# Kernel tuning notes

Hardware: AMD Instinct MI355X
Metric: run time of the kernel (lower is better)

Reference implementation:

```python
import jax, jax.numpy as jnp
import numpy as np

B_, L_, DM = 8, 1024, 256
DS, DC, EX = 16, 4, 2
DI = EX * DM            # d_inner = 512
DTR = max(1, DM // 16)  # dt_rank = 16


def setup_inputs() -> dict:
    key = jax.random.key(0)
    ks = iter(jax.random.split(key, 40))
    def n(shape, s=0.02):
        return jax.random.normal(next(ks), shape, jnp.float32) * s
    inp = {"x": jax.random.normal(next(ks), (B_, L_, DM), jnp.float32)}
    inp["norm_g"] = jnp.ones((DM,), jnp.float32)
    inp["norm_b"] = jnp.zeros((DM,), jnp.float32)
    for m in ("f", "b"):
        inp[f"inW_{m}"] = n((DM, 2 * DI))
        inp[f"convW_{m}"] = n((DI, DC))
        inp[f"convB_{m}"] = jnp.zeros((DI,), jnp.float32)
        inp[f"xW_{m}"] = n((DI, DTR + 2 * DS))
        inp[f"dtW_{m}"] = n((DTR, DI))
        inp[f"dtB_{m}"] = jnp.zeros((DI,), jnp.float32)
        # ALog init: log of [1..dState] repeated over dInner rows
        inp[f"ALog_{m}"] = jnp.log(jnp.tile(jnp.arange(1, DS + 1, dtype=jnp.float32), (DI, 1)))
        inp[f"Dp_{m}"] = jnp.ones((DI,), jnp.float32)
        inp[f"outW_{m}"] = n((DI, DM))
    inp["fusW"] = n((2 * DM, DM))
    inp["fusB"] = jnp.zeros((DM,), jnp.float32)
    return inp


def _dw_conv(x, w, b):
    # causal depthwise conv1d: x [B,L,DI], w [DI,DC] -> [B,L,DI]
    xc = jnp.transpose(x, (0, 2, 1))  # B,DI,L
    out = jax.lax.conv_general_dilated(
        xc, w[:, None, :], window_strides=(1,), padding=[(DC - 1, 0)],
        dimension_numbers=("NCH", "OIH", "NCH"), feature_group_count=DI)
    return jnp.transpose(out + b[:, None], (0, 2, 1))


def _ssm(x, xW, dtW, dtB, ALog, Dp):
    # x: [B,L,DI]
    A = -jnp.exp(ALog)                                   # [DI,DS]
    xdbl = x @ xW                                        # [B,L,DTR+2*DS]
    dlt, Bp, Cp = jnp.split(xdbl, [DTR, DTR + DS], axis=-1)
    delta = jax.nn.softplus(dlt @ dtW + dtB)             # [B,L,DI]
    dA = jnp.exp(delta[..., None] * A)                   # [B,L,DI,DS]
    dBx = (delta * x)[..., None] * Bp[:, :, None, :]     # [B,L,DI,DS]

    def step(h, t):
        a, bb, c = t
        h = a * h + bb                                   # [B,DI,DS]
        y = jnp.einsum('bdn,bn->bd', h, c)
        return h, y

    h0 = jnp.zeros((x.shape[0], DI, DS), x.dtype)
    _, ys = jax.lax.scan(step, h0, (jnp.moveaxis(dA, 1, 0),
                                    jnp.moveaxis(dBx, 1, 0),
                                    jnp.moveaxis(Cp, 1, 0)))
    return jnp.moveaxis(ys, 0, 1) + Dp * x               # [B,L,DI]


def _mamba(x, inW, convW, convB, xW, dtW, dtB, ALog, Dp, outW):
    xr = x @ inW                                         # [B,L,2*DI]
    xs, res = jnp.split(xr, 2, axis=-1)
    xs = jax.nn.silu(_dw_conv(xs, convW, convB))
    y = _ssm(xs, xW, dtW, dtB, ALog, Dp)
    return (y * jax.nn.silu(res)) @ outW                 # [B,L,DM]


def reference(x, norm_g, norm_b,
              inW_f, convW_f, convB_f, xW_f, dtW_f, dtB_f, ALog_f, Dp_f, outW_f,
              inW_b, convW_b, convB_b, xW_b, dtW_b, dtB_b, ALog_b, Dp_b, outW_b,
              fusW, fusB):
    # LayerNorm
    mu = x.mean(-1, keepdims=True)
    var = ((x - mu) ** 2).mean(-1, keepdims=True)
    xn = (x - mu) * jax.lax.rsqrt(var + 1e-5) * norm_g + norm_b
    # forward-direction Mamba
    xf = _mamba(xn, inW_f, convW_f, convB_f, xW_f, dtW_f, dtB_f, ALog_f, Dp_f, outW_f)
    # backward-direction Mamba (flip along time)
    xb = _mamba(jnp.flip(xn, 1), inW_b, convW_b, convB_b, xW_b, dtW_b, dtB_b, ALog_b, Dp_b, outW_b)
    xb = jnp.flip(xb, 1)
    fused = jnp.concatenate([xf, xb], axis=-1) @ fusW + fusB
    return x + fused  # dropout is identity in eval
```

## Files before the change

### kernel.cpp

```cpp
#include <hip/hip_runtime.h>
#include <cmath>

typedef __bf16 bf16x8 __attribute__((ext_vector_type(8)));
typedef float  f32x4  __attribute__((ext_vector_type(4)));
typedef float  f32x2  __attribute__((ext_vector_type(2)));

#define B_  8
#define L_  1024
#define DM  256
#define DI  512
#define DS  16
#define DTR 16
#define M_  (B_*L_)
#define NC  64
#define CT  16

__device__ inline float softplus_f(float z){
  return (z > 20.f) ? z : __logf(1.f + __expf(z));
}
__device__ inline float silu_f(float z){
  return z / (1.f + __expf(-z));
}

__device__ inline void pow_tree(float e1, float* p){
  float e2=e1*e1, e4=e2*e2, e8=e4*e4;
  float e3=e2*e1, e5=e4*e1, e6=e4*e2, e7=e4*e3;
  p[0]=e1;  p[1]=e2;  p[2]=e3;  p[3]=e4;
  p[4]=e5;  p[5]=e6;  p[6]=e7;  p[7]=e8;
  p[8]=e8*e1;  p[9]=e8*e2;  p[10]=e8*e3;  p[11]=e8*e4;
  p[12]=e8*e5; p[13]=e8*e6; p[14]=e8*e7;  p[15]=e8*e8;
}

__global__ __launch_bounds__(256) void probe_k(const void* x, int* flag){
  __shared__ int sbad[256];
  int tid = threadIdx.x;
  const unsigned short* u = (const unsigned short*)x;
  int bad = 0;
  for (int i = tid; i < 4096; i += 256){
    unsigned short v = u[2*i];
    int e = (v >> 7) & 0xFF;
    if (e >= 160 || e < 96) bad++;
  }
  sbad[tid] = bad;
  __syncthreads();
  if (tid == 0){
    int t = 0;
    for (int i=0;i<256;i++) t += sbad[i];
    *flag = (t > 1024) ? 1 : 0;
  }
}

struct CvtJob { const void* src; __bf16* dst; int n; };
struct CvtArgs { CvtJob j[11]; };

__global__ __launch_bounds__(256) void cvt_k(CvtArgs a, const int* flag){
  int e = blockIdx.x*256 + threadIdx.x;
  const int f = *flag;
  #pragma unroll 1
  for (int jj=0; jj<11; jj++){
    int n = a.j[jj].n;
    if (e < n){
      if (f) a.j[jj].dst[e] = (__bf16)(((const float*)a.j[jj].src)[e]);
      else   a.j[jj].dst[e] = ((const __bf16*)a.j[jj].src)[e];
      return;
    }
    e -= n;
  }
}

__global__ __launch_bounds__(256) void cvtA_k(const void* a0, const void* a1,
                                              float* o0, float* o1, const int* flag){
  int gid = blockIdx.x*256 + threadIdx.x;
  const int f = *flag;
  const void* src = (gid < 8192) ? a0 : a1;
  float* dst = (gid < 8192) ? o0 : o1;
  int i = gid & 8191;
  dst[i] = f ? ((const float*)src)[i] : (float)((const __bf16*)src)[i];
}

struct PrepJob { const void* src; void* dst; int rows; int cols; int f32out; };
struct PrepArgs { PrepJob j[11]; };

__global__ __launch_bounds__(256) void prep_k(PrepArgs a, const int* flag){
  int e = blockIdx.x*256 + threadIdx.x;
  const int f = *flag;
  #pragma unroll 1
  for (int jj=0; jj<11; jj++){
    int sz = a.j[jj].rows * a.j[jj].cols;
    if (e < sz){
      int cols = a.j[jj].cols;
      int r = e / cols, c = e - r*cols;
      float v = f ? ((const float*)a.j[jj].src)[e] : (float)((const __bf16*)a.j[jj].src)[e];
      if (a.j[jj].f32out) ((float*)a.j[jj].dst)[c*a.j[jj].rows + r] = v;
      else ((__bf16*)a.j[jj].dst)[(long)c*a.j[jj].rows + r] = (__bf16)v;
      return;
    }
    e -= sz;
  }
}

__global__ __launch_bounds__(256) void ln_k(const void* x, const __bf16* g,
                                            const __bf16* bb, __bf16* xn, const int* flag){
  const int row = blockIdx.x;
  const int d = threadIdx.x;
  const int f = *flag;
  long idx = (long)row*DM + d;
  float v = f ? ((const float*)x)[idx] : (float)(((const __bf16*)x)[idx]);
  float s = v, q = v*v;
  #pragma unroll
  for (int off=32; off>0; off>>=1){
    s += __shfl_down(s, off);
    q += __shfl_down(q, off);
  }
  __shared__ float ss[4], sq[4];
  int w = d >> 6, ln = d & 63;
  if (ln == 0){ ss[w] = s; sq[w] = q; }
  __syncthreads();
  s = ss[0]+ss[1]+ss[2]+ss[3];
  q = sq[0]+sq[1]+sq[2]+sq[3];
  float mu  = s * (1.f/DM);
  float var = q * (1.f/DM) - mu*mu;
  float xnv = (v - mu) * rsqrtf(var + 1e-5f) * (float)g[d] + (float)bb[d];
  xn[idx] = (__bf16)xnv;
}

template<int BM,int BN,int EPI,int KK>
__global__ __launch_bounds__(256) void gemm_lds_k(
    const __bf16* A0, const __bf16* A1,
    const __bf16* B0, const __bf16* B1,
    void* C0, void* C1,
    int lda, int ldb, int ldc,
    const __bf16* bias, const void* resid, const int* outflag)
{
  constexpr int TM = BM/2, TN = BN/2;
  constexpr int WMT = TM/16, WNT = TN/16;
  constexpr int LA = BM/64, LB = BN/64;

  const int dir = blockIdx.z;
  const __bf16* A  = dir ? A1 : A0;
  const __bf16* Bt = dir ? B1 : B0;
  char* C = (char*)(dir ? C1 : C0);
  __bf16* resW = (EPI==0) ? (__bf16*)(dir ? resid : (const void*)bias) : nullptr;
  const int tid  = threadIdx.x;
  const int lane = tid & 63;
  const int wid  = tid >> 6;
  const int wm = wid & 1;
  const int wn = wid >> 1;
  const int mBase = blockIdx.x * BM;
  const int nBase = blockIdx.y * BN;
  const int lm = lane & 15;
  const int kq = (lane >> 4) * 8;
  const int of = (EPI==3 && outflag) ? *outflag : 0;

  __shared__ __bf16 As[BM*32];
  __shared__ __bf16 Bs[BN*32];

  const __bf16* aS[LA];
  const __bf16* bS[LB];
  {
    int colk = (tid & 3) * 8;
    #pragma unroll
    for (int ld=0; ld<LA; ld++){
      int r = mBase + ld*64 + (tid >> 2);
      if (EPI==0 && dir==1){ int b = r >> 10, t = r & (L_-1); r = (b<<10) + (L_-1-t); }
      aS[ld] = A + (long)r*lda + colk;
    }
    #pragma unroll
    for (int ld=0; ld<LB; ld++){
      int r = nBase + ld*64 + (tid >> 2);
      bS[ld] = Bt + (long)r*ldb + colk;
    }
  }

  f32x4 acc[WMT][WNT] = {};
  for (int k0=0; k0<KK; k0+=32){
    #pragma unroll
    for (int ld=0; ld<LA; ld++)
      __builtin_amdgcn_global_load_lds(
        (const __attribute__((address_space(1))) void*)(aS[ld] + k0),
        (__attribute__((address_space(3))) void*)(&As[ld*2048 + tid*8]), 16, 0, 0);
    #pragma unroll
    for (int ld=0; ld<LB; ld++)
      __builtin_amdgcn_global_load_lds(
        (const __attribute__((address_space(1))) void*)(bS[ld] + k0),
        (__attribute__((address_space(3))) void*)(&Bs[ld*2048 + tid*8]), 16, 0, 0);
    __syncthreads();
    bf16x8 af[WMT], bfr[WNT];
    #pragma unroll
    for (int i=0;i<WMT;i++) af[i]  = *(const bf16x8*)&As[(wm*TM + i*16 + lm)*32 + kq];
    #pragma unroll
    for (int j=0;j<WNT;j++) bfr[j] = *(const bf16x8*)&Bs[(wn*TN + j*16 + lm)*32 + kq];
    #pragma unroll
    for (int i=0;i<WMT;i++)
      #pragma unroll
      for (int j=0;j<WNT;j++)
        acc[i][j] = __builtin_amdgcn_mfma_f32_16x16x32_bf16(af[i], bfr[j], acc[i][j], 0,0,0);
    __syncthreads();
  }

  const int coff = (EPI==2) ? dir*DM : 0;
  #pragma unroll
  for (int i=0;i<WMT;i++){
    #pragma unroll
    for (int rr=0;rr<4;rr++){
      int r = mBase + wm*TM + i*16 + (lane>>4)*4 + rr;
      int rOut = r;
      if (EPI==2 && dir==1){ int b = r >> 10, t = r & (L_-1); rOut = (b<<10) + (L_-1-t); }
      #pragma unroll
      for (int j=0;j<WNT;j++){
        int c = nBase + wn*TN + j*16 + lm;
        float v = acc[i][j][rr];
        if (EPI==0){
          if (c < DI) ((__bf16*)C)[(long)r*DI + c] = (__bf16)v;
          else        resW[(long)r*DI + (c-DI)]    = (__bf16)v;
        } else if (EPI==3){
          float rsd = of ? ((const float*)resid)[(long)r*DM + c]
                         : (float)((const __bf16*)resid)[(long)r*DM + c];
          v += (float)bias[c] + rsd;
          if (of) ((float*)C)[(long)r*ldc + c] = v;
          else    ((__bf16*)C)[(long)r*ldc + c] = (__bf16)v;
        } else {
          ((__bf16*)C)[(long)rOut*ldc + coff + c] = (__bf16)v;
        }
      }
    }
  }
}

template<int WMT,int WNT,int BWM,int BWN,int KK>
__global__ __launch_bounds__(64*BWM*BWN) void gemm_r_k(
    const __bf16* A0, const __bf16* A1,
    const __bf16* B0, const __bf16* B1,
    float* C0, float* C1,
    int lda, int ldb, int ldc)
{
  const int dir = blockIdx.z;
  const __bf16* A  = dir ? A1 : A0;
  const __bf16* Bt = dir ? B1 : B0;
  float* C = dir ? C1 : C0;
  const int tid  = threadIdx.x;
  const int lane = tid & 63;
  const int wid  = tid >> 6;
  const int wm = wid % BWM;
  const int wn = wid / BWM;
  const int mBase = (blockIdx.x*BWM + wm) * (WMT*16);
  const int nBase = (blockIdx.y*BWN + wn) * (WNT*16);
  const int lm = lane & 15;
  const int kq = (lane >> 4) * 8;

  long aoff[WMT];
  #pragma unroll
  for (int i=0;i<WMT;i++) aoff[i] = (long)(mBase + i*16 + lm) * lda + kq;
  long boff[WNT];
  #pragma unroll
  for (int j=0;j<WNT;j++) boff[j] = (long)(nBase + j*16 + lm) * ldb + kq;

  f32x4 acc[WMT][WNT] = {};
  #pragma unroll
  for (int k0=0; k0<KK; k0+=32){
    bf16x8 af[WMT], bfr[WNT];
    #pragma unroll
    for (int i=0;i<WMT;i++) af[i]  = *(const bf16x8*)(A  + aoff[i] + k0);
    #pragma unroll
    for (int j=0;j<WNT;j++) bfr[j] = *(const bf16x8*)(Bt + boff[j] + k0);
    #pragma unroll
    for (int i=0;i<WMT;i++)
      #pragma unroll
      for (int j=0;j<WNT;j++)
        acc[i][j] = __builtin_amdgcn_mfma_f32_16x16x32_bf16(af[i], bfr[j], acc[i][j], 0,0,0);
  }

  #pragma unroll
  for (int i=0;i<WMT;i++)
    #pragma unroll
    for (int rr=0;rr<4;rr++){
      int r = mBase + i*16 + (lane>>4)*4 + rr;
      #pragma unroll
      for (int j=0;j<WNT;j++){
        int c = nBase + j*16 + lm;
        C[(long)r*ldc + c] = acc[i][j][rr];
      }
    }
}

__global__ __launch_bounds__(256) void conv_k(
    const __bf16* xz0, const __bf16* xz1,
    const float* cw0, const float* cw1,
    const __bf16* cb0, const __bf16* cb1,
    __bf16* xs0, __bf16* xs1)
{
  const int dir = blockIdx.z;
  const __bf16* xz = dir ? xz1 : xz0;
  const float*  cw = dir ? cw1 : cw0;
  const __bf16* cb = dir ? cb1 : cb0;
  __bf16* xs = dir ? xs1 : xs0;

  int gid = blockIdx.x*256 + threadIdx.x;
  int c8 = gid & 63;
  int t  = (gid >> 6) & (L_-1);
  int b  = gid >> 16;
  int cbase = c8*8;

  float acc[8];
  bf16x8 bb = *(const bf16x8*)(cb + cbase);
  #pragma unroll
  for (int c=0;c<8;c++) acc[c] = (float)bb[c];
  #pragma unroll
  for (int j=0;j<4;j++){
    int tj = t - 3 + j;
    if (tj >= 0){
      bf16x8 xv = *(const bf16x8*)(xz + ((long)(b*L_ + tj))*DI + cbase);
      #pragma unroll
      for (int c=0;c<8;c++) acc[c] += (float)xv[c] * cw[j*DI + cbase + c];
    }
  }
  bf16x8 outv;
  #pragma unroll
  for (int c=0;c<8;c++) outv[c] = (__bf16)silu_f(acc[c]);
  *(bf16x8*)(xs + ((long)(b*L_ + t))*DI + cbase) = outv;
}

__global__ __launch_bounds__(256) void dt_k(
    const float* xd0, const float* xd1,
    const float* dw0, const float* dw1,
    const __bf16* dtB0, const __bf16* dtB1,
    float* dg0, float* dg1)
{
  const int dir = blockIdx.z;
  const float*  xd  = dir ? xd1 : xd0;
  const float*  dw  = dir ? dw1 : dw0;
  const __bf16* dtB = dir ? dtB1 : dtB0;
  float* dg = dir ? dg1 : dg0;
  const long row0 = (long)blockIdx.x * 32;
  const int tid = threadIdx.x;

  __shared__ float sdlt[32][16];
  { int e = tid*2; int r = e>>4, q = e&15;
    *(f32x2*)&sdlt[r][q] = *(const f32x2*)(xd + (row0+r)*48 + q); }

  const int d0 = tid, d1 = tid + 256;
  float dwa[16], dwb[16];
  { const f32x4* p = (const f32x4*)(dw + d0*DTR);
    #pragma unroll
    for (int q=0;q<4;q++){ f32x4 v=p[q]; dwa[q*4]=v[0]; dwa[q*4+1]=v[1]; dwa[q*4+2]=v[2]; dwa[q*4+3]=v[3]; } }
  { const f32x4* p = (const f32x4*)(dw + d1*DTR);
    #pragma unroll
    for (int q=0;q<4;q++){ f32x4 v=p[q]; dwb[q*4]=v[0]; dwb[q*4+1]=v[1]; dwb[q*4+2]=v[2]; dwb[q*4+3]=v[3]; } }
  const float b0v = (float)dtB[d0];
  const float b1v = (float)dtB[d1];
  __syncthreads();

  #pragma unroll 4
  for (int r=0;r<32;r++){
    f32x4 q0 = *(const f32x4*)&sdlt[r][0];
    f32x4 q1 = *(const f32x4*)&sdlt[r][4];
    f32x4 q2 = *(const f32x4*)&sdlt[r][8];
    f32x4 q3 = *(const f32x4*)&sdlt[r][12];
    float z0 = b0v, z1 = b1v;
    z0 += q0[0]*dwa[0]+q0[1]*dwa[1]+q0[2]*dwa[2]+q0[3]*dwa[3];
    z0 += q1[0]*dwa[4]+q1[1]*dwa[5]+q1[2]*dwa[6]+q1[3]*dwa[7];
    z0 += q2[0]*dwa[8]+q2[1]*dwa[9]+q2[2]*dwa[10]+q2[3]*dwa[11];
    z0 += q3[0]*dwa[12]+q3[1]*dwa[13]+q3[2]*dwa[14]+q3[3]*dwa[15];
    z1 += q0[0]*dwb[0]+q0[1]*dwb[1]+q0[2]*dwb[2]+q0[3]*dwb[3];
    z1 += q1[0]*dwb[4]+q1[1]*dwb[5]+q1[2]*dwb[6]+q1[3]*dwb[7];
    z1 += q2[0]*dwb[8]+q2[1]*dwb[9]+q2[2]*dwb[10]+q2[3]*dwb[11];
    z1 += q3[0]*dwb[12]+q3[1]*dwb[13]+q3[2]*dwb[14]+q3[3]*dwb[15];
    dg[(row0+r)*DI + d0] = softplus_f(z0);
    dg[(row0+r)*DI + d1] = softplus_f(z1);
  }
}

__global__ __launch_bounds__(256) void scanA_k(
    const float* xd0, const float* xd1,
    const __bf16* xs0, const __bf16* xs1,
    const float* dg0, const float* dg1,
    const float* ALf0, const float* ALf1,
    float* hend, float* sumd)
{
  const int dir = blockIdx.z;
  const float*  xd  = dir ? xd1 : xd0;
  const __bf16* xs  = dir ? xs1 : xs0;
  const float*  dg  = dir ? dg1 : dg0;
  const float*  ALf = dir ? ALf1 : ALf0;

  const int b   = blockIdx.y;
  const int c   = blockIdx.x >> 1;
  const int dg_ = blockIdx.x & 1;
  const int tid = threadIdx.x;
  const int d   = dg_*256 + tid;
  const int db  = dir*8 + b;
  const long row0 = (long)b*L_ + c*CT;

  __shared__ float sB[CT][16];
  if (tid < CT*4){ int e = tid*4; int t = e>>4, n = e&15;
    *(f32x4*)&sB[t][n] = *(const f32x4*)(xd + (row0+t)*48 + 16 + n); }

  float A[16];
  { const f32x4* p = (const f32x4*)(ALf + d*DS);
    #pragma unroll
    for (int q=0;q<4;q++){ f32x4 v=p[q];
      A[q*4]=-__expf(v[0]); A[q*4+1]=-__expf(v[1]); A[q*4+2]=-__expf(v[2]); A[q*4+3]=-__expf(v[3]); } }
  bool pow_ok = true;
  #pragma unroll
  for (int n=0;n<16;n++) pow_ok = pow_ok && (fabsf(A[n] + (float)(n+1)) < 0.003f*(n+1));

  float h[16];
  #pragma unroll
  for (int n=0;n<16;n++) h[n]=0.f;
  float sdelta = 0.f;
  __syncthreads();

  if (pow_ok){
    #pragma unroll 2
    for (int t=0;t<CT;t++){
      long row = row0 + t;
      f32x4 b0 = *(const f32x4*)&sB[t][0];
      f32x4 b1 = *(const f32x4*)&sB[t][4];
      f32x4 b2 = *(const f32x4*)&sB[t][8];
      f32x4 b3 = *(const f32x4*)&sB[t][12];
      float delta = dg[row*DI + d];
      sdelta += delta;
      float xv = (float)xs[row*DI + d];
      float dx = delta*xv;
      float pw[16];
      pow_tree(__expf(-delta), pw);
      float Bv[16] = {b0[0],b0[1],b0[2],b0[3], b1[0],b1[1],b1[2],b1[3],
                      b2[0],b2[1],b2[2],b2[3], b3[0],b3[1],b3[2],b3[3]};
      #pragma unroll
      for (int n=0;n<16;n++)
        h[n] = pw[n]*h[n] + dx*Bv[n];
    }
  } else {
    #pragma unroll 2
    for (int t=0;t<CT;t++){
      long row = row0 + t;
      f32x4 b0 = *(const f32x4*)&sB[t][0];
      f32x4 b1 = *(const f32x4*)&sB[t][4];
      f32x4 b2 = *(const f32x4*)&sB[t][8];
      f32x4 b3 = *(const f32x4*)&sB[t][12];
      float delta = dg[row*DI + d];
      sdelta += delta;
      float xv = (float)xs[row*DI + d];
      float dx = delta*xv;
      float Bv[16] = {b0[0],b0[1],b0[2],b0[3], b1[0],b1[1],b1[2],b1[3],
                      b2[0],b2[1],b2[2],b2[3], b3[0],b3[1],b3[2],b3[3]};
      #pragma unroll
      for (int n=0;n<16;n++)
        h[n] = __expf(delta*A[n])*h[n] + dx*Bv[n];
    }
  }

  long hb = (((long)db*NC + c)*DI + d)*16;
  f32x4* hp = (f32x4*)(hend + hb);
  #pragma unroll
  for (int q=0;q<4;q++){ f32x4 v; v[0]=h[q*4]; v[1]=h[q*4+1]; v[2]=h[q*4+2]; v[3]=h[q*4+3]; hp[q]=v; }
  sumd[((long)db*NC + c)*DI + d] = sdelta;
}

__global__ __launch_bounds__(256) void scanB_k(
    const float* ALf0, const float* ALf1,
    const float* hend, const float* sumd, float* Hbuf)
{
  int gid = blockIdx.x*256 + threadIdx.x;
  int n  = gid & 15;
  int d  = (gid>>4) & 511;
  int db = gid >> 13;
  const float* ALf = (db>=8) ? ALf1 : ALf0;
  float A_dn = -__expf(ALf[d*DS + n]);
  float H = 0.f;
  #pragma unroll 1
  for (int c=0;c<NC;c++){
    long base = (((long)db*NC + c)*DI + d)*16 + n;
    Hbuf[base] = H;
    float S = sumd[((long)db*NC + c)*DI + d];
    H = hend[base] + __expf(A_dn*S)*H;
  }
}

__global__ __launch_bounds__(256) void scanC_k(
    const float* xd0, const float* xd1,
    const __bf16* xs0, const __bf16* xs1,
    __bf16* res0, __bf16* res1,
    const float* dg0, const float* dg1,
    const float* ALf0, const float* ALf1,
    const __bf16* Dp0, const __bf16* Dp1,
    const float* Hbuf)
{
  const int dir = blockIdx.z;
  const float*  xd  = dir ? xd1 : xd0;
  const __bf16* xs  = dir ? xs1 : xs0;
  __bf16*       res = dir ? res1 : res0;
  const float*  dg  = dir ? dg1 : dg0;
  const float*  ALf = dir ? ALf1 : ALf0;
  const __bf16* Dp  = dir ? Dp1 : Dp0;

  const int b   = blockIdx.y;
  const int c   = blockIdx.x >> 1;
  const int dg_ = blockIdx.x & 1;
  const int tid = threadIdx.x;
  const int d   = dg_*256 + tid;
  const int db  = dir*8 + b;
  const long row0 = (long)b*L_ + c*CT;

  __shared__ float sBC[CT][32];
  if (tid < CT*8){ int e = tid*4; int t = e>>5, cc = e&31;
    *(f32x4*)&sBC[t][cc] = *(const f32x4*)(xd + (row0+t)*48 + 16 + cc); }

  float A[16];
  { const f32x4* p = (const f32x4*)(ALf + d*DS);
    #pragma unroll
    for (int q=0;q<4;q++){ f32x4 v=p[q];
      A[q*4]=-__expf(v[0]); A[q*4+1]=-__expf(v[1]); A[q*4+2]=-__expf(v[2]); A[q*4+3]=-__expf(v[3]); } }
  bool pow_ok = true;
  #pragma unroll
  for (int n=0;n<16;n++) pow_ok = pow_ok && (fabsf(A[n] + (float)(n+1)) < 0.003f*(n+1));

  float h[16];
  { long hb = (((long)db*NC + c)*DI + d)*16;
    const f32x4* p = (const f32x4*)(Hbuf + hb);
    #pragma unroll
    for (int q=0;q<4;q++){ f32x4 v = p[q]; h[q*4]=v[0]; h[q*4+1]=v[1]; h[q*4+2]=v[2]; h[q*4+3]=v[3]; } }
  const float Dpv = (float)Dp[d];
  __syncthreads();

  if (pow_ok){
    #pragma unroll 2
    for (int t=0;t<CT;t++){
      long row = row0 + t;
      f32x4 b0 = *(const f32x4*)&sBC[t][0];
      f32x4 b1 = *(const f32x4*)&sBC[t][4];
      f32x4 b2 = *(const f32x4*)&sBC[t][8];
      f32x4 b3 = *(const f32x4*)&sBC[t][12];
      f32x4 c0 = *(const f32x4*)&sBC[t][16];
      f32x4 c1 = *(const f32x4*)&sBC[t][20];
      f32x4 c2 = *(const f32x4*)&sBC[t][24];
      f32x4 c3 = *(const f32x4*)&sBC[t][28];
      float delta = dg[row*DI + d];
      float xv = (float)xs[row*DI + d];
      float dx = delta*xv;
      float pw[16];
      pow_tree(__expf(-delta), pw);
      float Bv[16] = {b0[0],b0[1],b0[2],b0[3], b1[0],b1[1],b1[2],b1[3],
                      b2[0],b2[1],b2[2],b2[3], b3[0],b3[1],b3[2],b3[3]};
      float Cv[16] = {c0[0],c0[1],c0[2],c0[3], c1[0],c1[1],c1[2],c1[3],
                      c2[0],c2[1],c2[2],c2[3], c3[0],c3[1],c3[2],c3[3]};
      float p = 0.f;
      #pragma unroll
      for (int n=0;n<16;n++){
        h[n] = pw[n]*h[n] + dx*Bv[n];
        p += h[n]*Cv[n];
      }
      float yv = p + Dpv*xv;
      float rv = (float)res[row*DI + d];
      res[row*DI + d] = (__bf16)(yv * silu_f(rv));
    }
  } else {
    #pragma unroll 2
    for (int t=0;t<CT;t++){
      long row = row0 + t;
      f32x4 b0 = *(const f32x4*)&sBC[t][0];
      f32x4 b1 = *(const f32x4*)&sBC[t][4];
      f32x4 b2 = *(const f32x4*)&sBC[t][8];
      f32x4 b3 = *(const f32x4*)&sBC[t][12];
      f32x4 c0 = *(const f32x4*)&sBC[t][16];
      f32x4 c1 = *(const f32x4*)&sBC[t][20];
      f32x4 c2 = *(const f32x4*)&sBC[t][24];
      f32x4 c3 = *(const f32x4*)&sBC[t][28];
      float delta = dg[row*DI + d];
      float xv = (float)xs[row*DI + d];
      float dx = delta*xv;
      float Bv[16] = {b0[0],b0[1],b0[2],b0[3], b1[0],b1[1],b1[2],b1[3],
                      b2[0],b2[1],b2[2],b2[3], b3[0],b3[1],b3[2],b3[3]};
      float Cv[16] = {c0[0],c0[1],c0[2],c0[3], c1[0],c1[1],c1[2],c1[3],
                      c2[0],c2[1],c2[2],c2[3], c3[0],c3[1],c3[2],c3[3]};
      float p = 0.f;
      #pragma unroll
      for (int n=0;n<16;n++){
        h[n] = __expf(delta*A[n])*h[n] + dx*Bv[n];
        p += h[n]*Cv[n];
      }
      float yv = p + Dpv*xv;
      float rv = (float)res[row*DI + d];
      res[row*DI + d] = (__bf16)(yv * silu_f(rv));
    }
  }
}

__global__ __launch_bounds__(256) void scan_k(
    const float* xd0, const float* xd1,
    const __bf16* xs0, const __bf16* xs1,
    __bf16* res0, __bf16* res1,
    const float* dw0, const float* dw1,
    const __bf16* dtB0, const __bf16* dtB1,
    const __bf16* AL0, const __bf16* AL1,
    const __bf16* Dp0, const __bf16* Dp1)
{
  const int dir = blockIdx.z;
  const float*  xd  = dir ? xd1 : xd0;
  const __bf16* xs  = dir ? xs1 : xs0;
  __bf16*       res = dir ? res1 : res0;
  const float*  dw  = dir ? dw1 : dw0;
  const __bf16* dtB = dir ? dtB1 : dtB0;
  const __bf16* AL  = dir ? AL1 : AL0;
  const __bf16* Dp  = dir ? Dp1 : Dp0;

  const int b  = blockIdx.y;
  const int dt = blockIdx.x;
  const int tid = threadIdx.x;
  const int n  = tid & 15;
  const int dl = tid >> 4;
  const int d  = dt*16 + dl;

  __shared__ float sxd[128][48];
  __shared__ float sx[128][16];
  __shared__ float sdelta[128][16];
  __shared__ float sy[128][16];
  __shared__ float sdw[16][17];
  __shared__ float sdb[16];

  sdw[dl][n] = dw[(dt*16+dl)*DTR + n];
  if (tid < 16) sdb[tid] = (float)dtB[dt*16 + tid];
  const float A_dn = -__expf((float)AL[d*DS + n]);
  float h = 0.f;
  __syncthreads();

  const long rowB = (long)b * L_;
  for (int c0=0; c0<L_; c0+=128){
    #pragma unroll 1
    for (int k=0;k<24;k++){
      int e = tid + k*256;
      int t = e / 48, col = e - t*48;
      sxd[t][col] = xd[(rowB + c0 + t)*48 + col];
    }
    #pragma unroll 1
    for (int k=0;k<8;k++){
      int e = tid + k*256;
      int t = e >> 4, dc = e & 15;
      sx[t][dc] = (float)xs[(rowB + c0 + t)*DI + dt*16 + dc];
    }
    __syncthreads();
    #pragma unroll 1
    for (int k=0;k<8;k++){
      int e = tid + k*256;
      int t = e >> 4, dc = e & 15;
      float z = sdb[dc];
      #pragma unroll
      for (int q=0;q<16;q++) z += sxd[t][q] * sdw[dc][q];
      sdelta[t][dc] = softplus_f(z);
    }
    __syncthreads();
    #pragma unroll 2
    for (int tt=0;tt<128;tt++){
      float delta = sdelta[tt][dl];
      float xv = sx[tt][dl];
      float Bv = sxd[tt][16+n];
      float Cv = sxd[tt][32+n];
      float dA = __expf(delta * A_dn);
      h = dA*h + (delta*xv)*Bv;
      float p = h * Cv;
      p += __shfl_xor(p, 1);
      p += __shfl_xor(p, 2);
      p += __shfl_xor(p, 4);
      p += __shfl_xor(p, 8);
      if (n == 0) sy[tt][dl] = p;
    }
    __syncthreads();
    #pragma unroll 1
    for (int k=0;k<8;k++){
      int e = tid + k*256;
      int t = e >> 4, dc = e & 15;
      long row = rowB + c0 + t;
      float yv = sy[t][dc] + (float)Dp[dt*16+dc] * sx[t][dc];
      float rv = (float)res[row*DI + dt*16 + dc];
      res[row*DI + dt*16 + dc] = (__bf16)(yv * silu_f(rv));
    }
    __syncthreads();
  }
}

extern "C" void kernel_launch(void* const* d_in, const int* in_sizes, int n_in,
                              void* d_out, int out_size, void* d_ws, size_t ws_size,
                              hipStream_t stream)
{
  const size_t MB = 1u<<20;
  if (ws_size < 61*MB) return;
  const bool newscan = (ws_size >= 160*MB);

  char* w = (char*)d_ws;
  __bf16* xz[2]  = {(__bf16*)(w + 0),      (__bf16*)(w + 8*MB)};
  __bf16* res[2] = {(__bf16*)(w + 16*MB),  (__bf16*)(w + 24*MB)};
  __bf16* xsc[2] = {(__bf16*)(w + 32*MB),  (__bf16*)(w + 40*MB)};
  __bf16* xn     = (__bf16*)(w + 48*MB);
  float*  xdbl[2]= {(float*)(w + 48*MB),   (float*)(w + 48*MB + (size_t)M_*48*4)};
  __bf16* fusedIn = xsc[0];

  char* wp = w + 52*MB;
  auto carve = [&](size_t bytes)->void*{
    void* p = wp;
    wp += (bytes + 255) & ~(size_t)255;
    return p;
  };
  __bf16 *inWt[2], *xWt[2], *outWt[2];
  float *dtWt[2], *convWt[2];
  for (int m=0;m<2;m++){
    inWt[m]   = (__bf16*)carve((size_t)(2*DI)*DM*2);
    xWt[m]    = (__bf16*)carve((size_t)48*DI*2);
    outWt[m]  = (__bf16*)carve((size_t)DM*DI*2);
    dtWt[m]   = (float*)carve((size_t)DI*DTR*4);
    convWt[m] = (float*)carve((size_t)4*DI*4);
  }
  __bf16* fusWt = (__bf16*)carve((size_t)DM*DI*2);
  int* flag = (int*)carve(256);
  float* ALf[2] = {(float*)carve((size_t)DI*DS*4), (float*)carve((size_t)DI*DS*4)};

  char* cp = w + 55*MB;
  auto carve2 = [&](size_t elems)->__bf16*{
    __bf16* p = (__bf16*)cp;
    cp += (elems*2 + 255) & ~(size_t)255;
    return p;
  };
  __bf16* ngc = carve2(DM);
  __bf16* nbc = carve2(DM);
  __bf16 *convBc[2], *dtBc[2], *ALc[2], *Dpc[2];
  for (int m=0;m<2;m++){
    convBc[m] = carve2(DI);
    dtBc[m]   = carve2(DI);
    ALc[m]    = carve2((size_t)DI*DS);
    Dpc[m]    = carve2(DI);
  }
  __bf16* fusBc = carve2(DM);

  float* dgA[2] = {(float*)(w + 56*MB), (float*)(w + 72*MB)};
  float* hend = (float*)(w + 88*MB);
  float* sumd = (float*)(w + 122*MB);
  float* Hbuf = (float*)(w + 125*MB);

  probe_k<<<1, 256, 0, stream>>>(d_in[0], flag);

  CvtArgs ca;
  int ci = 0;
  ca.j[ci++] = {d_in[1],  ngc, DM};
  ca.j[ci++] = {d_in[2],  nbc, DM};
  for (int m=0;m<2;m++){
    int base = 3 + m*9;
    ca.j[ci++] = {d_in[base+2], convBc[m], DI};
    ca.j[ci++] = {d_in[base+5], dtBc[m],   DI};
    ca.j[ci++] = {d_in[base+6], ALc[m],    DI*DS};
    ca.j[ci++] = {d_in[base+7], Dpc[m],    DI};
  }
  ca.j[ci++] = {d_in[22], fusBc, DM};
  cvt_k<<<79, 256, 0, stream>>>(ca, flag);
  cvtA_k<<<64, 256, 0, stream>>>(d_in[9], d_in[18], ALf[0], ALf[1], flag);

  PrepArgs pa;
  int ji = 0;
  for (int m=0;m<2;m++){
    int base = 3 + m*9;
    pa.j[ji++] = {d_in[base+0], inWt[m],  DM,  2*DI, 0};
    pa.j[ji++] = {d_in[base+3], xWt[m],   DI,  48,   0};
    pa.j[ji++] = {d_in[base+8], outWt[m], DI,  DM,   0};
    pa.j[ji++] = {d_in[base+4], dtWt[m],  DTR, DI,   1};
    pa.j[ji++] = {d_in[base+1], convWt[m],DI,  4,    1};
  }
  pa.j[ji++] = {d_in[21], fusWt, DI, DM, 0};
  prep_k<<<(987136+255)/256, 256, 0, stream>>>(pa, flag);

  ln_k<<<M_, 256, 0, stream>>>(d_in[0], ngc, nbc, xn, flag);
  gemm_lds_k<128,128,0,256><<<dim3(M_/128, (2*DI)/128, 2), 256, 0, stream>>>(
      xn, xn, inWt[0], inWt[1], xz[0], xz[1], DM, DM, DI, res[0], res[1], nullptr);
  conv_k<<<dim3((M_*64)/256, 1, 2), 256, 0, stream>>>(
      xz[0], xz[1], convWt[0], convWt[1], convBc[0], convBc[1], xsc[0], xsc[1]);
  gemm_r_k<1,3,4,1,512><<<dim3(M_/64, 1, 2), 256, 0, stream>>>(
      xsc[0], xsc[1], xWt[0], xWt[1], xdbl[0], xdbl[1], DI, DI, 48);

  if (newscan){
    dt_k<<<dim3(M_/32, 1, 2), 256, 0, stream>>>(
        xdbl[0], xdbl[1], dtWt[0], dtWt[1], dtBc[0], dtBc[1], dgA[0], dgA[1]);
    scanA_k<<<dim3(NC*2, B_, 2), 256, 0, stream>>>(
        xdbl[0], xdbl[1], xsc[0], xsc[1], dgA[0], dgA[1], ALf[0], ALf[1], hend, sumd);
    scanB_k<<<131072/256, 256, 0, stream>>>(ALf[0], ALf[1], hend, sumd, Hbuf);
    scanC_k<<<dim3(NC*2, B_, 2), 256, 0, stream>>>(
        xdbl[0], xdbl[1], xsc[0], xsc[1], res[0], res[1],
        dgA[0], dgA[1], ALf[0], ALf[1], Dpc[0], Dpc[1], Hbuf);
  } else {
    scan_k<<<dim3(DI/16, B_, 2), 256, 0, stream>>>(
        xdbl[0], xdbl[1], xsc[0], xsc[1], res[0], res[1], dtWt[0], dtWt[1],
        dtBc[0], dtBc[1], ALc[0], ALc[1], Dpc[0], Dpc[1]);
  }

  gemm_lds_k<64,64,2,512><<<dim3(M_/64, DM/64, 2), 256, 0, stream>>>(
      res[0], res[1], outWt[0], outWt[1], fusedIn, fusedIn, DI, DI, 2*DM, nullptr, nullptr, nullptr);
  gemm_lds_k<64,64,3,512><<<dim3(M_/64, DM/64, 1), 256, 0, stream>>>(
      fusedIn, fusedIn, fusWt, fusWt, d_out, d_out, 2*DM, 2*DM, DM, fusBc, d_in[0], flag);
}
```

Baseline: 286.3 us.

## Fold out-projection into fusion weights and merge conversion kernels

Precomputes the product of each direction's out-projection with its half of the fusion weight (outW·fusW) using a small GEMM. The final stage then becomes a single GEMM that accumulates both directions' gated SSM outputs over K=512 each against the combined weights, with the backward direction's time flip handled at load. This removes the intermediate fusedIn tensor and one large GEMM launch. The separate cvt/cvtA kernels are folded into the generalized prep kernel. The combined weights are rounded to bf16, which changes numerics slightly.

After: 283.4 us. No clear change (-1.0%).

```diff
diff --git a/kernel.cpp b/kernel.cpp
--- a/kernel.cpp
+++ b/kernel.cpp
@@ -50,42 +50,14 @@
   }
 }
 
-struct CvtJob { const void* src; __bf16* dst; int n; };
-struct CvtArgs { CvtJob j[11]; };
-
-__global__ __launch_bounds__(256) void cvt_k(CvtArgs a, const int* flag){
-  int e = blockIdx.x*256 + threadIdx.x;
-  const int f = *flag;
-  #pragma unroll 1
-  for (int jj=0; jj<11; jj++){
-    int n = a.j[jj].n;
-    if (e < n){
-      if (f) a.j[jj].dst[e] = (__bf16)(((const float*)a.j[jj].src)[e]);
-      else   a.j[jj].dst[e] = ((const __bf16*)a.j[jj].src)[e];
-      return;
-    }
-    e -= n;
-  }
-}
-
-__global__ __launch_bounds__(256) void cvtA_k(const void* a0, const void* a1,
-                                              float* o0, float* o1, const int* flag){
-  int gid = blockIdx.x*256 + threadIdx.x;
-  const int f = *flag;
-  const void* src = (gid < 8192) ? a0 : a1;
-  float* dst = (gid < 8192) ? o0 : o1;
-  int i = gid & 8191;
-  dst[i] = f ? ((const float*)src)[i] : (float)((const __bf16*)src)[i];
-}
-
 struct PrepJob { const void* src; void* dst; int rows; int cols; int f32out; };
-struct PrepArgs { PrepJob j[11]; };
+struct PrepArgs { PrepJob j[26]; int nj; };
 
 __global__ __launch_bounds__(256) void prep_k(PrepArgs a, const int* flag){
   int e = blockIdx.x*256 + threadIdx.x;
   const int f = *flag;
   #pragma unroll 1
-  for (int jj=0; jj<11; jj++){
+  for (int jj=0; jj<a.nj; jj++){
     int sz = a.j[jj].rows * a.j[jj].cols;
     if (e < sz){
       int cols = a.j[jj].cols;
@@ -124,23 +96,20 @@
   xn[idx] = (__bf16)xnv;
 }
 
-template<int BM,int BN,int EPI,int KK>
-__global__ __launch_bounds__(256) void gemm_lds_k(
-    const __bf16* A0, const __bf16* A1,
-    const __bf16* B0, const __bf16* B1,
-    void* C0, void* C1,
-    int lda, int ldb, int ldc,
-    const __bf16* bias, const void* resid, const int* outflag)
+template<int BM,int BN,int KK>
+__global__ __launch_bounds__(256) void gemm_in_k(
+    const __bf16* A, const __bf16* B0, const __bf16* B1,
+    __bf16* xz0, __bf16* xz1, __bf16* res0, __bf16* res1,
+    int lda, int ldb)
 {
   constexpr int TM = BM/2, TN = BN/2;
   constexpr int WMT = TM/16, WNT = TN/16;
   constexpr int LA = BM/64, LB = BN/64;
 
   const int dir = blockIdx.z;
-  const __bf16* A  = dir ? A1 : A0;
   const __bf16* Bt = dir ? B1 : B0;
-  char* C = (char*)(dir ? C1 : C0);
-  __bf16* resW = (EPI==0) ? (__bf16*)(dir ? resid : (const void*)bias) : nullptr;
+  __bf16* xz  = dir ? xz1 : xz0;
+  __bf16* res = dir ? res1 : res0;
   const int tid  = threadIdx.x;
   const int lane = tid & 63;
   const int wid  = tid >> 6;
@@ -150,7 +119,6 @@
   const int nBase = blockIdx.y * BN;
   const int lm = lane & 15;
   const int kq = (lane >> 4) * 8;
-  const int of = (EPI==3 && outflag) ? *outflag : 0;
 
   __shared__ __bf16 As[BM*32];
   __shared__ __bf16 Bs[BN*32];
@@ -162,7 +130,7 @@
     #pragma unroll
     for (int ld=0; ld<LA; ld++){
       int r = mBase + ld*64 + (tid >> 2);
-      if (EPI==0 && dir==1){ int b = r >> 10, t = r & (L_-1); r = (b<<10) + (L_-1-t); }
+      if (dir==1){ int b = r >> 10, t = r & (L_-1); r = (b<<10) + (L_-1-t); }
       aS[ld] = A + (long)r*lda + colk;
     }
     #pragma unroll
@@ -198,46 +166,123 @@
     __syncthreads();
   }
 
-  const int coff = (EPI==2) ? dir*DM : 0;
   #pragma unroll
   for (int i=0;i<WMT;i++){
     #pragma unroll
     for (int rr=0;rr<4;rr++){
       int r = mBase + wm*TM + i*16 + (lane>>4)*4 + rr;
-      int rOut = r;
-      if (EPI==2 && dir==1){ int b = r >> 10, t = r & (L_-1); rOut = (b<<10) + (L_-1-t); }
       #pragma unroll
       for (int j=0;j<WNT;j++){
         int c = nBase + wn*TN + j*16 + lm;
         float v = acc[i][j][rr];
-        if (EPI==0){
-          if (c < DI) ((__bf16*)C)[(long)r*DI + c] = (__bf16)v;
-          else        resW[(long)r*DI + (c-DI)]    = (__bf16)v;
-        } else if (EPI==3){
-          float rsd = of ? ((const float*)resid)[(long)r*DM + c]
-                         : (float)((const __bf16*)resid)[(long)r*DM + c];
-          v += (float)bias[c] + rsd;
-          if (of) ((float*)C)[(long)r*ldc + c] = v;
-          else    ((__bf16*)C)[(long)r*ldc + c] = (__bf16)v;
-        } else {
-          ((__bf16*)C)[(long)rOut*ldc + coff + c] = (__bf16)v;
-        }
+        if (c < DI) xz[(long)r*DI + c] = (__bf16)v;
+        else        res[(long)r*DI + (c-DI)] = (__bf16)v;
       }
     }
   }
 }
 
-template<int WMT,int WNT,int BWM,int BWN,int KK>
+template<int BM,int BN,int KK>
+__global__ __launch_bounds__(256) void gemm_fin_k(
+    const __bf16* Af, const __bf16* Ab,
+    const __bf16* Bt0, const __bf16* Bt1,
+    void* Cout, const __bf16* bias, const void* resid, const int* outflag)
+{
+  constexpr int TM = BM/2, TN = BN/2;
+  constexpr int WMT = TM/16, WNT = TN/16;
+  constexpr int LA = BM/64, LB = BN/64;
+
+  const int tid  = threadIdx.x;
+  const int lane = tid & 63;
+  const int wid  = tid >> 6;
+  const int wm = wid & 1;
+  const int wn = wid >> 1;
+  const int mBase = blockIdx.x * BM;
+  const int nBase = blockIdx.y * BN;
+  const int lm = lane & 15;
+  const int kq = (lane >> 4) * 8;
+  const int of = outflag ? *outflag : 0;
+
+  __shared__ __bf16 As[BM*32];
+  __shared__ __bf16 Bs[BN*32];
+
+  f32x4 acc[WMT][WNT] = {};
+  #pragma unroll 1
+  for (int dd=0; dd<2; dd++){
+    const __bf16* A  = dd ? Ab  : Af;
+    const __bf16* Bt = dd ? Bt1 : Bt0;
+    const __bf16* aS[LA];
+    const __bf16* bS[LB];
+    {
+      int colk = (tid & 3) * 8;
+      #pragma unroll
+      for (int ld=0; ld<LA; ld++){
+        int r = mBase + ld*64 + (tid >> 2);
+        if (dd==1){ int b = r >> 10, t = r & (L_-1); r = (b<<10) + (L_-1-t); }
+        aS[ld] = A + (long)r*DI + colk;
+      }
+      #pragma unroll
+      for (int ld=0; ld<LB; ld++){
+        int r = nBase + ld*64 + (tid >> 2);
+        bS[ld] = Bt + (long)r*DI + colk;
+      }
+    }
+    for (int k0=0; k0<KK; k0+=32){
+      #pragma unroll
+      for (int ld=0; ld<LA; ld++)
+        __builtin_amdgcn_global_load_lds(
+          (const __attribute__((address_space(1))) void*)(aS[ld] + k0),
+          (__attribute__((address_space(3))) void*)(&As[ld*2048 + tid*8]), 16, 0, 0);
+      #pragma unroll
+      for (int ld=0; ld<LB; ld++)
+        __builtin_amdgcn_global_load_lds(
+          (const __attribute__((address_space(1))) void*)(bS[ld] + k0),
+          (__attribute__((address_space(3))) void*)(&Bs[ld*2048 + tid*8]), 16, 0, 0);
+      __syncthreads();
+      bf16x8 af[WMT], bfr[WNT];
+      #pragma unroll
+      for (int i=0;i<WMT;i++) af[i]  = *(const bf16x8*)&As[(wm*TM + i*16 + lm)*32 + kq];
+      #pragma unroll
+      for (int j=0;j<WNT;j++) bfr[j] = *(const bf16x8*)&Bs[(wn*TN + j*16 + lm)*32 + kq];
+      #pragma unroll
+      for (int i=0;i<WMT;i++)
+        #pragma unroll
+        for (int j=0;j<WNT;j++)
+          acc[i][j] = __builtin_amdgcn_mfma_f32_16x16x32_bf16(af[i], bfr[j], acc[i][j], 0,0,0);
+      __syncthreads();
+    }
+  }
+
+  #pragma unroll
+  for (int i=0;i<WMT;i++){
+    #pragma unroll
+    for (int rr=0;rr<4;rr++){
+      int r = mBase + wm*TM + i*16 + (lane>>4)*4 + rr;
+      #pragma unroll
+      for (int j=0;j<WNT;j++){
+        int c = nBase + wn*TN + j*16 + lm;
+        float v = acc[i][j][rr];
+        float rsd = of ? ((const float*)resid)[(long)r*DM + c]
+                       : (float)((const __bf16*)resid)[(long)r*DM + c];
+        v += (float)bias[c] + rsd;
+        if (of) ((float*)Cout)[(long)r*DM + c] = v;
+        else    ((__bf16*)Cout)[(long)r*DM + c] = (__bf16)v;
+      }
+    }
+  }
+}
+
+template<int WMT,int WNT,int BWM,int BWN,int KK,int BF16OUT>
 __global__ __launch_bounds__(64*BWM*BWN) void gemm_r_k(
     const __bf16* A0, const __bf16* A1,
     const __bf16* B0, const __bf16* B1,
-    float* C0, float* C1,
+    void* C0, void* C1,
     int lda, int ldb, int ldc)
 {
   const int dir = blockIdx.z;
   const __bf16* A  = dir ? A1 : A0;
   const __bf16* Bt = dir ? B1 : B0;
-  float* C = dir ? C1 : C0;
+  void* C = dir ? C1 : C0;
   const int tid  = threadIdx.x;
   const int lane = tid & 63;
   const int wid  = tid >> 6;
@@ -278,7 +323,8 @@
       #pragma unroll
       for (int j=0;j<WNT;j++){
         int c = nBase + j*16 + lm;
-        C[(long)r*ldc + c] = acc[i][j][rr];
+        if (BF16OUT) ((__bf16*)C)[(long)r*ldc + c] = (__bf16)acc[i][j][rr];
+        else         ((float*)C)[(long)r*ldc + c] = acc[i][j][rr];
       }
     }
 }
@@ -692,7 +738,6 @@
   __bf16* xsc[2] = {(__bf16*)(w + 32*MB),  (__bf16*)(w + 40*MB)};
   __bf16* xn     = (__bf16*)(w + 48*MB);
   float*  xdbl[2]= {(float*)(w + 48*MB),   (float*)(w + 48*MB + (size_t)M_*48*4)};
-  __bf16* fusedIn = xsc[0];
 
   char* wp = w + 52*MB;
   auto carve = [&](size_t bytes)->void*{
@@ -700,20 +745,21 @@
     wp += (bytes + 255) & ~(size_t)255;
     return p;
   };
-  __bf16 *inWt[2], *xWt[2], *outWt[2];
+  __bf16 *inWt[2], *xWt[2], *outWr[2], *BtC[2];
   float *dtWt[2], *convWt[2];
   for (int m=0;m<2;m++){
     inWt[m]   = (__bf16*)carve((size_t)(2*DI)*DM*2);
     xWt[m]    = (__bf16*)carve((size_t)48*DI*2);
-    outWt[m]  = (__bf16*)carve((size_t)DM*DI*2);
+    outWr[m]  = (__bf16*)carve((size_t)DI*DM*2);
+    BtC[m]    = (__bf16*)carve((size_t)DM*DI*2);
     dtWt[m]   = (float*)carve((size_t)DI*DTR*4);
     convWt[m] = (float*)carve((size_t)4*DI*4);
   }
-  __bf16* fusWt = (__bf16*)carve((size_t)DM*DI*2);
+  __bf16* fusWt = (__bf16*)carve((size_t)DM*(2*DM)*2);
   int* flag = (int*)carve(256);
   float* ALf[2] = {(float*)carve((size_t)DI*DS*4), (float*)carve((size_t)DI*DS*4)};
 
-  char* cp = w + 55*MB;
+  char* cp = w + 57*MB;
   auto carve2 = [&](size_t elems)->__bf16*{
     __bf16* p = (__bf16*)cp;
     cp += (elems*2 + 255) & ~(size_t)255;
@@ -730,47 +776,50 @@
   }
   __bf16* fusBc = carve2(DM);
 
-  float* dgA[2] = {(float*)(w + 56*MB), (float*)(w + 72*MB)};
-  float* hend = (float*)(w + 88*MB);
-  float* sumd = (float*)(w + 122*MB);
-  float* Hbuf = (float*)(w + 125*MB);
+  float* dgA[2] = {(float*)(w + 58*MB), (float*)(w + 74*MB)};
+  float* hend = (float*)(w + 90*MB);
+  float* sumd = (float*)(w + 124*MB);
+  float* Hbuf = (float*)(w + 127*MB);
 
   probe_k<<<1, 256, 0, stream>>>(d_in[0], flag);
 
-  CvtArgs ca;
-  int ci = 0;
-  ca.j[ci++] = {d_in[1],  ngc, DM};
-  ca.j[ci++] = {d_in[2],  nbc, DM};
+  PrepArgs pa;
+  int ji = 0;
+  size_t tot = 0;
+  auto addj = [&](const void* s, void* dst, int rows, int cols, int f32o){
+    pa.j[ji++] = {s, dst, rows, cols, f32o};
+    tot += (size_t)rows*cols;
+  };
   for (int m=0;m<2;m++){
     int base = 3 + m*9;
-    ca.j[ci++] = {d_in[base+2], convBc[m], DI};
-    ca.j[ci++] = {d_in[base+5], dtBc[m],   DI};
-    ca.j[ci++] = {d_in[base+6], ALc[m],    DI*DS};
-    ca.j[ci++] = {d_in[base+7], Dpc[m],    DI};
-  }
-  ca.j[ci++] = {d_in[22], fusBc, DM};
-  cvt_k<<<79, 256, 0, stream>>>(ca, flag);
-  cvtA_k<<<64, 256, 0, stream>>>(d_in[9], d_in[18], ALf[0], ALf[1], flag);
-
-  PrepArgs pa;
-  int ji = 0;
-  for (int m=0;m<2;m++){
-    int base = 3 + m*9;
-    pa.j[ji++] = {d_in[base+0], inWt[m],  DM,  2*DI, 0};
-    pa.j[ji++] = {d_in[base+3], xWt[m],   DI,  48,   0};
-    pa.j[ji++] = {d_in[base+8], outWt[m], DI,  DM,   0};
-    pa.j[ji++] = {d_in[base+4], dtWt[m],  DTR, DI,   1};
-    pa.j[ji++] = {d_in[base+1], convWt[m],DI,  4,    1};
-  }
-  pa.j[ji++] = {d_in[21], fusWt, DI, DM, 0};
-  prep_k<<<(987136+255)/256, 256, 0, stream>>>(pa, flag);
+    addj(d_in[base+0], inWt[m],  DM,  2*DI, 0);
+    addj(d_in[base+3], xWt[m],   DI,  48,   0);
+    addj(d_in[base+8], outWr[m], 1,   DI*DM,0);
+    addj(d_in[base+4], dtWt[m],  DTR, DI,   1);
+    addj(d_in[base+1], convWt[m],DI,  4,    1);
+    addj(d_in[base+2], convBc[m],1, DI, 0);
+    addj(d_in[base+5], dtBc[m],  1, DI, 0);
+    addj(d_in[base+6], ALc[m],   1, DI*DS, 0);
+    addj(d_in[base+6], (void*)ALf[m], 1, DI*DS, 1);
+    addj(d_in[base+7], Dpc[m],   1, DI, 0);
+  }
+  addj(d_in[21], fusWt, 2*DM, DM, 0);
+  addj(d_in[1],  ngc, 1, DM, 0);
+  addj(d_in[2],  nbc, 1, DM, 0);
+  addj(d_in[22], fusBc, 1, DM, 0);
+  pa.nj = ji;
+  prep_k<<<(int)((tot+255)/256), 256, 0, stream>>>(pa, flag);
+
+  gemm_r_k<1,4,4,1,DM,1><<<dim3(4, 8, 2), 256, 0, stream>>>(
+      fusWt, fusWt + DM,
+      outWr[0], outWr[1], BtC[0], BtC[1], 2*DM, DM, DI);
 
   ln_k<<<M_, 256, 0, stream>>>(d_in[0], ngc, nbc, xn, flag);
-  gemm_lds_k<128,128,0,256><<<dim3(M_/128, (2*DI)/128, 2), 256, 0, stream>>>(
-      xn, xn, inWt[0], inWt[1], xz[0], xz[1], DM, DM, DI, res[0], res[1], nullptr);
+  gemm_in_k<128,128,256><<<dim3(M_/128, (2*DI)/128, 2), 256, 0, stream>>>(
+      xn, inWt[0], inWt[1], xz[0], xz[1], res[0], res[1], DM, DM);
   conv_k<<<dim3((M_*64)/256, 1, 2), 256, 0, stream>>>(
       xz[0], xz[1], convWt[0], convWt[1], convBc[0], convBc[1], xsc[0], xsc[1]);
-  gemm_r_k<1,3,4,1,512><<<dim3(M_/64, 1, 2), 256, 0, stream>>>(
+  gemm_r_k<1,3,4,1,DI,0><<<dim3(M_/64, 1, 2), 256, 0, stream>>>(
       xsc[0], xsc[1], xWt[0], xWt[1], xdbl[0], xdbl[1], DI, DI, 48);
 
   if (newscan){
@@ -788,8 +837,6 @@
         dtBc[0], dtBc[1], ALc[0], ALc[1], Dpc[0], Dpc[1]);
   }
 
-  gemm_lds_k<64,64,2,512><<<dim3(M_/64, DM/64, 2), 256, 0, stream>>>(
-      res[0], res[1], outWt[0], outWt[1], fusedIn, fusedIn, DI, DI, 2*DM, nullptr, nullptr, nullptr);
-  gemm_lds_k<64,64,3,512><<<dim3(M_/64, DM/64, 1), 256, 0, stream>>>(
-      fusedIn, fusedIn, fusWt, fusWt, d_out, d_out, 2*DM, 2*DM, DM, fusBc, d_in[0], flag);
-}
+  gemm_fin_k<64,64,DI><<<dim3(M_/64, DM/64, 1), 256, 0, stream>>>(
+      res[0], res[1], BtC[0], BtC[1], d_out, fusBc, d_in[0], flag);
+}
```
